# Performance work log

Hardware: AMD Instinct MI355X
Metric: run time of the kernel (lower is better)

## Reference

```python
import jax, jax.numpy as jnp
import numpy as np

N = 8192
IN_F = 512
OUT_F = 128
NUM_CLASSES = 10
ALPHA = 0.2  # LeakyReLU negative slope
NEG_INF = -9e15


def setup_inputs() -> dict:
    key = jax.random.key(0)
    k_h, k_d, k_W, k_a, k_cw, k_cb = jax.random.split(key, 6)
    h = jax.random.normal(k_h, (N, IN_F), dtype=jnp.float32)
    dist = jax.random.randint(k_d, (N, N), 0, 2, dtype=jnp.int32)
    # xavier_uniform with gain=1.414
    gain = 1.414
    lim_W = gain * np.sqrt(6.0 / (IN_F + OUT_F))
    W = jax.random.uniform(k_W, (IN_F, OUT_F), minval=-lim_W, maxval=lim_W, dtype=jnp.float32)
    lim_a = gain * np.sqrt(6.0 / (2 * OUT_F + 1))
    a = jax.random.uniform(k_a, (2 * OUT_F, 1), minval=-lim_a, maxval=lim_a, dtype=jnp.float32)
    # nn.Linear(out_features, num_classes): weight [C, out], bias [C]
    lim_c = np.sqrt(1.0 / OUT_F)
    Wc = jax.random.uniform(k_cw, (NUM_CLASSES, OUT_F), minval=-lim_c, maxval=lim_c, dtype=jnp.float32)
    bc = jax.random.uniform(k_cb, (NUM_CLASSES,), minval=-lim_c, maxval=lim_c, dtype=jnp.float32)
    return {"h": h, "dist": dist, "W": W, "a": a, "Wc": Wc, "bc": bc}


def reference(h, dist, W, a, Wc, bc):
    Wh = h @ W                              # [N, out]
    Wh1 = Wh @ a[:OUT_F]                    # [N, 1]
    Wh2 = Wh @ a[OUT_F:]                    # [N, 1]
    e = jax.nn.leaky_relu(Wh1 + Wh2.T, negative_slope=ALPHA)  # [N, N]
    att = jnp.where(dist > 0, e, NEG_INF)
    att = jax.nn.softmax(att, axis=1)       # [N, N]
    h_update = jax.nn.elu(att @ Wh)         # [N, out] (dropout inactive at inference)
    y_pred = h_update @ Wc.T + bc           # [N, num_classes]
    return y_pred
```

## Files before the change

### kernel.cpp

```cpp
#include <hip/hip_runtime.h>
#include <stdint.h>

#define N 8192
#define IN_F 512
#define OUT_F 128
#define NCLS 10
#define ALPHA 0.2f

typedef float f32x4 __attribute__((ext_vector_type(4)));
typedef int   i32x4 __attribute__((ext_vector_type(4)));
typedef short s16x4 __attribute__((ext_vector_type(4)));
typedef short s16x8 __attribute__((ext_vector_type(8)));

__device__ __forceinline__ short f2bf(float x) {
    unsigned u = __builtin_bit_cast(unsigned, x);
    u = (u + 0x7FFFu + ((u >> 16) & 1u)) >> 16;
    return (short)u;
}
__device__ __forceinline__ float bf2f(short s) {
    unsigned u = ((unsigned)(unsigned short)s) << 16;
    return __builtin_bit_cast(float, u);
}

__global__ __launch_bounds__(256, 8)
void mask_kernel(const int* __restrict__ dist, unsigned* __restrict__ mask) {
    size_t w = (size_t)blockIdx.x * 256 + threadIdx.x;
    const int* p = dist + w * 32;
    unsigned b = 0;
    #pragma unroll
    for (int u = 0; u < 8; ++u) {
        i32x4 v = *(const i32x4*)(p + u * 4);
        #pragma unroll
        for (int e = 0; e < 4; ++e) b |= (v[e] > 0 ? 1u : 0u) << (u * 4 + e);
    }
    mask[w] = b;
}

__global__ void split_w_kernel(const float* __restrict__ W,
                               short* __restrict__ WThi, short* __restrict__ WTlo) {
    int idx = blockIdx.x * 256 + threadIdx.x;
    int k = idx >> 7, col = idx & 127;
    float x = W[idx];
    short hi = f2bf(x);
    short lo = f2bf(x - bf2f(hi));
    size_t a = (size_t)(k >> 5) * (128 * 32) + (size_t)col * 32 + (k & 31);
    WThi[a] = hi;
    WTlo[a] = lo;
}

#define WH_ROWS 16
#define WH_STR 520

__global__ __launch_bounds__(256, 2)
void wh_kernel(const float* __restrict__ h, const short* __restrict__ WThi,
               const short* __restrict__ WTlo, const float* __restrict__ a,
               short* __restrict__ WhT, float* __restrict__ Wh1,
               float* __restrict__ Wh2) {
    __shared__ __align__(16) short Ahi[WH_ROWS][WH_STR];
    __shared__ __align__(16) short Alo[WH_ROWS][WH_STR];
    __shared__ __align__(16) float whs[WH_ROWS][OUT_F + 4];

    const int t = threadIdx.x;
    const int r0 = blockIdx.x * WH_ROWS;

    {
        int row = t >> 4, c4 = t & 15;
        const float* hrow = h + (size_t)(r0 + row) * IN_F;
        #pragma unroll
        for (int jj = 0; jj < 4; ++jj) {
            int k0 = c4 * 8 + jj * 128;
            f32x4 x0 = *(const f32x4*)(hrow + k0);
            f32x4 x1 = *(const f32x4*)(hrow + k0 + 4);
            s16x8 hi, lo;
            #pragma unroll
            for (int e = 0; e < 4; ++e) {
                short h0 = f2bf(x0[e]); hi[e] = h0; lo[e] = f2bf(x0[e] - bf2f(h0));
                short h1 = f2bf(x1[e]); hi[4 + e] = h1; lo[4 + e] = f2bf(x1[e] - bf2f(h1));
            }
            *(s16x8*)&Ahi[row][k0] = hi;
            *(s16x8*)&Alo[row][k0] = lo;
        }
    }
    __syncthreads();

    const int lane = t & 63, w = t >> 6;
    const int q = lane >> 4, ln16 = lane & 15;
    f32x4 acc[2] = {};
    #pragma unroll
    for (int kc = 0; kc < IN_F / 32; ++kc) {
        s16x8 ahi = *(const s16x8*)&Ahi[ln16][kc * 32 + q * 8];
        s16x8 alo = *(const s16x8*)&Alo[ln16][kc * 32 + q * 8];
        #pragma unroll
        for (int nt = 0; nt < 2; ++nt) {
            int col = w * 32 + nt * 16 + ln16;
            size_t boff = (size_t)kc * 4096 + (size_t)col * 32 + q * 8;
            s16x8 bhi = *(const s16x8*)(WThi + boff);
            s16x8 blo = *(const s16x8*)(WTlo + boff);
            acc[nt] = __builtin_amdgcn_mfma_f32_16x16x32_bf16(ahi, bhi, acc[nt], 0, 0, 0);
            acc[nt] = __builtin_amdgcn_mfma_f32_16x16x32_bf16(ahi, blo, acc[nt], 0, 0, 0);
            acc[nt] = __builtin_amdgcn_mfma_f32_16x16x32_bf16(alo, bhi, acc[nt], 0, 0, 0);
        }
    }
    #pragma unroll
    for (int nt = 0; nt < 2; ++nt)
        #pragma unroll
        for (int reg = 0; reg < 4; ++reg)
            whs[q * 4 + reg][w * 32 + nt * 16 + ln16] = acc[nt][reg];
    __syncthreads();

    if (t < 128) {
        int r = t >> 3, s = t & 7;
        float s1 = 0.f, s2 = 0.f;
        #pragma unroll
        for (int cc = 0; cc < 16; ++cc) {
            int c = s * 16 + cc;
            float v = whs[r][c];
            s1 = fmaf(v, a[c], s1);
            s2 = fmaf(v, a[OUT_F + c], s2);
        }
        s1 += __shfl_xor(s1, 1); s1 += __shfl_xor(s1, 2); s1 += __shfl_xor(s1, 4);
        s2 += __shfl_xor(s2, 1); s2 += __shfl_xor(s2, 2); s2 += __shfl_xor(s2, 4);
        if (s == 0) { Wh1[r0 + r] = s1; Wh2[r0 + r] = s2; }
    }

    {
        int c = t >> 1, h8 = t & 1;
        s16x8 pack;
        #pragma unroll
        for (int rr = 0; rr < 8; ++rr) pack[rr] = f2bf(whs[h8 * 8 + rr][c]);
        size_t addr = (size_t)(r0 >> 5) * 4096 + (size_t)c * 32 + (r0 & 16) + h8 * 8;
        *(s16x8*)(WhT + addr) = pack;
    }
}

#define BM2 64

__global__ __launch_bounds__(256, 4)
void attn_kernel(const unsigned* __restrict__ mask, const short* __restrict__ WhT,
                 const float* __restrict__ Wh1v, const float* __restrict__ Wh2v,
                 float* __restrict__ acc_part, float* __restrict__ l_part,
                 int nkc, int jspan) {
    const int t = threadIdx.x;
    const int it = blockIdx.x & 127;
    const int sp = blockIdx.x >> 7;
    const int i0 = it * BM2;
    const int w = t >> 6, lane = t & 63;
    const int q = lane >> 4, ln16 = lane & 15;
    const int row = i0 + w * 16 + ln16;
    const int j0 = sp * jspan;

    const unsigned* __restrict__ mp = mask + (size_t)row * (N / 32) + (j0 >> 5);
    const float* __restrict__ wp = Wh2v + j0 + q * 8;
    const float wh1 = Wh1v[row];
    const short* __restrict__ wb0 = WhT + ((size_t)(j0 >> 5)) * 4096 + ln16 * 32 + q * 8;

    f32x4 acc[8] = {};
    float l_acc = 0.f;

    unsigned mw = mp[0];
    f32x4 wA = *(const f32x4*)(wp);
    f32x4 wB = *(const f32x4*)(wp + 4);

    for (int kc = 0; kc < nkc; ++kc) {
        unsigned mw2 = 0; f32x4 wA2, wB2;
        const bool more = (kc + 1) < nkc;
        if (more) {
            mw2 = mp[kc + 1];
            wA2 = *(const f32x4*)(wp + (kc + 1) * 32);
            wB2 = *(const f32x4*)(wp + (kc + 1) * 32 + 4);
        }
        const unsigned byte = mw >> (q * 8);
        s16x8 af;
        #pragma unroll
        for (int e = 0; e < 4; ++e) {
            float sv = wh1 + wA[e];
            float lr = fmaxf(sv, ALPHA * sv);
            float pv = (byte & (1u << e)) ? __expf(lr) : 0.f;
            l_acc += pv;
            af[e] = f2bf(pv);
        }
        #pragma unroll
        for (int e = 0; e < 4; ++e) {
            float sv = wh1 + wB[e];
            float lr = fmaxf(sv, ALPHA * sv);
            float pv = (byte & (1u << (4 + e))) ? __expf(lr) : 0.f;
            l_acc += pv;
            af[4 + e] = f2bf(pv);
        }
        const short* wb = wb0 + (size_t)kc * 4096;
        #pragma unroll
        for (int nt = 0; nt < 8; ++nt) {
            s16x8 b = *(const s16x8*)(wb + nt * 512);
            acc[nt] = __builtin_amdgcn_mfma_f32_16x16x32_bf16(af, b, acc[nt], 0, 0, 0);
        }
        if (more) { mw = mw2; wA = wA2; wB = wB2; }
    }

    l_acc += __shfl_xor(l_acc, 16);
    l_acc += __shfl_xor(l_acc, 32);
    if (lane < 16) l_part[(size_t)sp * N + row] = l_acc;

    float* ap = acc_part + (size_t)sp * N * OUT_F + (size_t)(i0 + w * 16) * OUT_F;
    #pragma unroll
    for (int reg = 0; reg < 4; ++reg) {
        int rr = q * 4 + reg;
        #pragma unroll
        for (int nt = 0; nt < 8; ++nt)
            ap[(size_t)rr * OUT_F + nt * 16 + ln16] = acc[nt][reg];
    }
}

__global__ __launch_bounds__(256, 4)
void reduce_kernel(const float* __restrict__ acc_part, const float* __restrict__ l_part,
                   const float* __restrict__ Wc, const float* __restrict__ bcv,
                   float* __restrict__ out, int split) {
    __shared__ __align__(16) float hu[16][OUT_F + 4];
    const int t = threadIdx.x;
    const int i0 = blockIdx.x * 16;
    const int row = t >> 4, cg = t & 15;

    f32x4 v0 = {0.f, 0.f, 0.f, 0.f}, v1 = {0.f, 0.f, 0.f, 0.f};
    float l = 0.f;
    for (int s = 0; s < split; ++s) {
        const float* ap = acc_part + (size_t)s * N * OUT_F + (size_t)(i0 + row) * OUT_F + cg * 8;
        v0 += *(const f32x4*)ap;
        v1 += *(const f32x4*)(ap + 4);
        l += l_part[(size_t)s * N + i0 + row];
    }
    float inv = 1.f / l;
    #pragma unroll
    for (int e = 0; e < 4; ++e) {
        float x0 = v0[e] * inv; x0 = x0 > 0.f ? x0 : (__expf(x0) - 1.f);
        float x1 = v1[e] * inv; x1 = x1 > 0.f ? x1 : (__expf(x1) - 1.f);
        hu[row][cg * 8 + e] = x0;
        hu[row][cg * 8 + 4 + e] = x1;
    }
    __syncthreads();

    if (t < 16 * NCLS) {
        int rr = t / NCLS, cls = t - rr * NCLS;
        const f32x4* hurow = (const f32x4*)&hu[rr][0];
        const f32x4* wcrow = (const f32x4*)(Wc + cls * OUT_F);
        float sum = bcv[cls];
        #pragma unroll 8
        for (int c4 = 0; c4 < OUT_F / 4; ++c4) {
            f32x4 hv = hurow[c4];
            f32x4 wv = wcrow[c4];
            sum += hv[0] * wv[0] + hv[1] * wv[1] + hv[2] * wv[2] + hv[3] * wv[3];
        }
        out[(size_t)(i0 + rr) * NCLS + cls] = sum;
    }
}

extern "C" void kernel_launch(void* const* d_in, const int* in_sizes, int n_in,
                              void* d_out, int out_size, void* d_ws, size_t ws_size,
                              hipStream_t stream) {
    const float* h    = (const float*)d_in[0];
    const int*   dist = (const int*)d_in[1];
    const float* W    = (const float*)d_in[2];
    const float* a    = (const float*)d_in[3];
    const float* Wc   = (const float*)d_in[4];
    const float* bc   = (const float*)d_in[5];
    float* out = (float*)d_out;

    char* ws = (char*)d_ws;
    size_t off = 0;
    short* WhT  = (short*)(ws + off); off += (size_t)OUT_F * N * 2;
    short* WThi = (short*)(ws + off); off += (size_t)IN_F * OUT_F * 2;
    short* WTlo = (short*)(ws + off); off += (size_t)IN_F * OUT_F * 2;
    float* Wh1  = (float*)(ws + off); off += (size_t)N * 4;
    float* Wh2  = (float*)(ws + off); off += (size_t)N * 4;
    unsigned* mask = (unsigned*)(ws + off); off += (size_t)N * (N / 32) * 4;

    size_t per_split = (size_t)N * OUT_F * 4 + (size_t)N * 4;
    int split = 8;
    while (split > 1 && off + (size_t)split * per_split > ws_size) split >>= 1;
    float* acc_part = (float*)(ws + off); off += (size_t)split * N * OUT_F * 4;
    float* l_part   = (float*)(ws + off);

    hipLaunchKernelGGL(mask_kernel, dim3(N * (N / 32) / 256), dim3(256), 0, stream,
                       dist, mask);
    hipLaunchKernelGGL(split_w_kernel, dim3(256), dim3(256), 0, stream, W, WThi, WTlo);
    hipLaunchKernelGGL(wh_kernel, dim3(N / WH_ROWS), dim3(256), 0, stream,
                       h, WThi, WTlo, a, WhT, Wh1, Wh2);
    hipLaunchKernelGGL(attn_kernel, dim3(128 * split), dim3(256), 0, stream,
                       mask, WhT, Wh1, Wh2, acc_part, l_part,
                       N / (32 * split), N / split);
    hipLaunchKernelGGL(reduce_kernel, dim3(N / 16), dim3(256), 0, stream,
                       acc_part, l_part, Wc, bc, out, split);
}
```

Baseline: 479.9 us.

## Stage Wh2 in LDS, preload row mask words, fully unroll attention loop

Fixes the key split at 8 as a compile-time constant so the attention loop can be fully unrolled. Each block stages its Wh2 slice in shared memory, and each thread loads all of its row's mask words up front with vector loads, repacking the byte for its quad. Block index mapping is swapped so the 8 splits of the same row tile run adjacently, which may improve L2 reuse of mask and WhT. The cost is more registers for the mask bytes and the unrolled body, plus dropping the fallback that lowered the split when workspace is small.

Measured after the change: 473.0 us. No clear change (-1.4%).

```diff
diff --git a/kernel.cpp b/kernel.cpp
--- a/kernel.cpp
+++ b/kernel.cpp
@@ -134,42 +134,54 @@
 }
 
 #define BM2 64
+#define SPLIT 8
+#define NKC (N / (32 * SPLIT))
+#define JSPAN (N / SPLIT)
 
 __global__ __launch_bounds__(256, 4)
 void attn_kernel(const unsigned* __restrict__ mask, const short* __restrict__ WhT,
                  const float* __restrict__ Wh1v, const float* __restrict__ Wh2v,
-                 float* __restrict__ acc_part, float* __restrict__ l_part,
-                 int nkc, int jspan) {
+                 float* __restrict__ acc_part, float* __restrict__ l_part) {
+    __shared__ __align__(16) float wh2s[JSPAN];
+
     const int t = threadIdx.x;
-    const int it = blockIdx.x & 127;
-    const int sp = blockIdx.x >> 7;
+    const int sp = blockIdx.x & 7;
+    const int it = blockIdx.x >> 3;
     const int i0 = it * BM2;
     const int w = t >> 6, lane = t & 63;
     const int q = lane >> 4, ln16 = lane & 15;
     const int row = i0 + w * 16 + ln16;
-    const int j0 = sp * jspan;
+    const int j0 = sp * JSPAN;
+
+    *(f32x4*)&wh2s[t * 4] = *(const f32x4*)(Wh2v + j0 + t * 4);
 
     const unsigned* __restrict__ mp = mask + (size_t)row * (N / 32) + (j0 >> 5);
-    const float* __restrict__ wp = Wh2v + j0 + q * 8;
+    unsigned mb[8];
+    #pragma unroll
+    for (int u = 0; u < 8; ++u) {
+        i32x4 m = *(const i32x4*)(mp + u * 4);
+        unsigned b0 = ((unsigned)m[0] >> (q * 8)) & 255u;
+        unsigned b1 = ((unsigned)m[1] >> (q * 8)) & 255u;
+        unsigned b2 = ((unsigned)m[2] >> (q * 8)) & 255u;
+        unsigned b3 = ((unsigned)m[3] >> (q * 8)) & 255u;
+        mb[u] = b0 | (b1 << 8) | (b2 << 16) | (b3 << 24);
+    }
+
     const float wh1 = Wh1v[row];
-    const short* __restrict__ wb0 = WhT + ((size_t)(j0 >> 5)) * 4096 + ln16 * 32 + q * 8;
+    const short* __restrict__ wb0 =
+        WhT + ((size_t)(j0 >> 5)) * 4096 + ln16 * 32 + q * 8;
 
     f32x4 acc[8] = {};
     float l_acc = 0.f;
 
-    unsigned mw = mp[0];
-    f32x4 wA = *(const f32x4*)(wp);
-    f32x4 wB = *(const f32x4*)(wp + 4);
-
-    for (int kc = 0; kc < nkc; ++kc) {
-        unsigned mw2 = 0; f32x4 wA2, wB2;
-        const bool more = (kc + 1) < nkc;
-        if (more) {
-            mw2 = mp[kc + 1];
-            wA2 = *(const f32x4*)(wp + (kc + 1) * 32);
-            wB2 = *(const f32x4*)(wp + (kc + 1) * 32 + 4);
-        }
-        const unsigned byte = mw >> (q * 8);
+    __syncthreads();
+
+    #pragma unroll
+    for (int kc = 0; kc < NKC; ++kc) {
+        const unsigned byte = (mb[kc >> 2] >> ((kc & 3) * 8)) & 255u;
+        const float* wsrc = &wh2s[kc * 32 + q * 8];
+        f32x4 wA = *(const f32x4*)(wsrc);
+        f32x4 wB = *(const f32x4*)(wsrc + 4);
         s16x8 af;
         #pragma unroll
         for (int e = 0; e < 4; ++e) {
@@ -193,7 +205,6 @@
             s16x8 b = *(const s16x8*)(wb + nt * 512);
             acc[nt] = __builtin_amdgcn_mfma_f32_16x16x32_bf16(af, b, acc[nt], 0, 0, 0);
         }
-        if (more) { mw = mw2; wA = wA2; wB = wB2; }
     }
 
     l_acc += __shfl_xor(l_acc, 16);
@@ -272,10 +283,7 @@
     float* Wh2  = (float*)(ws + off); off += (size_t)N * 4;
     unsigned* mask = (unsigned*)(ws + off); off += (size_t)N * (N / 32) * 4;
 
-    size_t per_split = (size_t)N * OUT_F * 4 + (size_t)N * 4;
-    int split = 8;
-    while (split > 1 && off + (size_t)split * per_split > ws_size) split >>= 1;
-    float* acc_part = (float*)(ws + off); off += (size_t)split * N * OUT_F * 4;
+    float* acc_part = (float*)(ws + off); off += (size_t)SPLIT * N * OUT_F * 4;
     float* l_part   = (float*)(ws + off);
 
     hipLaunchKernelGGL(mask_kernel, dim3(N * (N / 32) / 256), dim3(256), 0, stream,
@@ -283,9 +291,8 @@
     hipLaunchKernelGGL(split_w_kernel, dim3(256), dim3(256), 0, stream, W, WThi, WTlo);
     hipLaunchKernelGGL(wh_kernel, dim3(N / WH_ROWS), dim3(256), 0, stream,
                        h, WThi, WTlo, a, WhT, Wh1, Wh2);
-    hipLaunchKernelGGL(attn_kernel, dim3(128 * split), dim3(256), 0, stream,
-                       mask, WhT, Wh1, Wh2, acc_part, l_part,
-                       N / (32 * split), N / split);
+    hipLaunchKernelGGL(attn_kernel, dim3(128 * SPLIT), dim3(256), 0, stream,
+                       mask, WhT, Wh1, Wh2, acc_part, l_part);
     hipLaunchKernelGGL(reduce_kernel, dim3(N / 16), dim3(256), 0, stream,
-                       acc_part, l_part, Wc, bc, out, split);
-}
+                       acc_part, l_part, Wc, bc, out, SPLIT);
+}
```
